# Kernel optimization log

Hardware: AMD Instinct MI355X
Metric: run time of the kernel (lower is better)

## Reference

```python
import jax, jax.numpy as jnp
import numpy as np

VOCAB = 30522
H = 100
T, B = 256, 16


def _lstm(x, W_ih, W_hh, b_ih, b_hh):
    # x: [T, B, I]; PyTorch gate order: i, f, g, o stacked in 4H rows.
    gx = jnp.einsum('tbi,gi->tbg', x, W_ih) + b_ih + b_hh  # [T, B, 4H]
    Hd = W_hh.shape[1]
    h0 = jnp.zeros((x.shape[1], Hd), x.dtype)
    c0 = jnp.zeros((x.shape[1], Hd), x.dtype)

    def step(carry, g_t):
        h, c = carry
        gates = g_t + h @ W_hh.T
        i, f, g, o = jnp.split(gates, 4, axis=-1)
        c = jax.nn.sigmoid(f) * c + jax.nn.sigmoid(i) * jnp.tanh(g)
        h = jax.nn.sigmoid(o) * jnp.tanh(c)
        return (h, c), h

    (h, c), hs = jax.lax.scan(step, (h0, c0), gx)
    return hs, (h, c)


def setup_inputs() -> dict:
    key = jax.random.key(0)
    ks = jax.random.split(key, 12)
    s = 1.0 / np.sqrt(H)
    u = lambda k, shp: jax.random.uniform(k, shp, jnp.float32, -s, s)
    return {
        'input': jax.random.randint(ks[0], (T, B), 0, VOCAB),
        'emb': jax.random.normal(ks[1], (VOCAB, H), jnp.float32),
        'enc_W_ih': u(ks[2], (4 * H, H)),
        'enc_W_hh': u(ks[3], (4 * H, H)),
        'enc_b_ih': u(ks[4], (4 * H,)),
        'enc_b_hh': u(ks[5], (4 * H,)),
        'dec_W_ih': u(ks[6], (4 * H, H)),
        'dec_W_hh': u(ks[7], (4 * H, H)),
        'dec_b_ih': u(ks[8], (4 * H,)),
        'dec_b_hh': u(ks[9], (4 * H,)),
        'out_W': u(ks[10], (VOCAB, H)),
        'out_b': u(ks[11], (VOCAB,)),
    }


def reference(input, emb, enc_W_ih, enc_W_hh, enc_b_ih, enc_b_hh,
              dec_W_ih, dec_W_hh, dec_b_ih, dec_b_hh, out_W, out_b):
    embedded = emb[input]  # [T, B, H]
    # Encoder is run in the original forward but its (hidden, cell) are unused.
    _hs, (_h, _c) = _lstm(embedded, enc_W_ih, enc_W_hh, enc_b_ih, enc_b_hh)
    dec_out, _ = _lstm(embedded, dec_W_ih, dec_W_hh, dec_b_ih, dec_b_hh)
    out = jnp.einsum('tbh,vh->tbv', dec_out, out_W) + out_b  # [T, B, VOCAB]
    return out
```

## Files before the change

kernel.cpp:

```cpp
#include <hip/hip_runtime.h>

#define HH 100
#define G4 400
#define TT 256
#define BB 16
#define TB 4096
#define VV 30522
#define GX_ROWS 8
#define PR 64

__global__ void k_tw_ih(const float* __restrict__ W, float* __restrict__ Wt) {
    int idx = blockIdx.x * blockDim.x + threadIdx.x;
    if (idx < G4 * HH) {
        int j = idx / HH, k = idx - j * HH;
        Wt[k * G4 + j] = W[idx];
    }
}

__global__ void k_tw_out(const float* __restrict__ W, float* __restrict__ Wt) {
    int v = blockIdx.x * blockDim.x + threadIdx.x;
    if (v < VV) {
        #pragma unroll 4
        for (int k = 0; k < HH; ++k) Wt[(long)k * VV + v] = W[(long)v * HH + k];
    }
}

__global__ __launch_bounds__(256) void k_gx(const int* __restrict__ tok,
                                            const float* __restrict__ emb,
                                            const float* __restrict__ WtIh,
                                            const float* __restrict__ bih,
                                            const float* __restrict__ bhh,
                                            float* __restrict__ gx) {
    __shared__ float x_s[GX_ROWS * HH];
    int tid = threadIdx.x;
    int row0 = blockIdx.x * GX_ROWS;
    for (int i = tid; i < GX_ROWS * HH; i += 256) {
        int r = i / HH, k = i - r * HH;
        x_s[i] = emb[(long)tok[row0 + r] * HH + k];
    }
    __syncthreads();
    for (int j = tid; j < G4; j += 256) {
        float bias = bih[j] + bhh[j];
        float acc[GX_ROWS];
        #pragma unroll
        for (int r = 0; r < GX_ROWS; ++r) acc[r] = bias;
        for (int k = 0; k < HH; ++k) {
            float w = WtIh[k * G4 + j];
            #pragma unroll
            for (int r = 0; r < GX_ROWS; ++r) acc[r] += w * x_s[r * HH + k];
        }
        #pragma unroll
        for (int r = 0; r < GX_ROWS; ++r) gx[(long)(row0 + r) * G4 + j] = acc[r];
    }
}

__global__ __launch_bounds__(512) void k_lstm(const float* __restrict__ gx,
                                              const float* __restrict__ Whh,
                                              float* __restrict__ dec) {
    __shared__ float h_s[HH];
    __shared__ float gates_s[G4];
    int tid = threadIdx.x;
    int b = blockIdx.x;
    float w[HH];
    if (tid < G4) {
        #pragma unroll
        for (int k = 0; k < HH; ++k) w[k] = Whh[tid * HH + k];
    }
    float c = 0.f;
    if (tid < HH) h_s[tid] = 0.f;
    __syncthreads();
    for (int t = 0; t < TT; ++t) {
        int row = t * BB + b;
        if (tid < G4) {
            float gxv = gx[(long)row * G4 + tid];
            float a0 = 0.f, a1 = 0.f, a2 = 0.f, a3 = 0.f;
            #pragma unroll
            for (int k = 0; k < HH; k += 4) {
                a0 += w[k]     * h_s[k];
                a1 += w[k + 1] * h_s[k + 1];
                a2 += w[k + 2] * h_s[k + 2];
                a3 += w[k + 3] * h_s[k + 3];
            }
            gates_s[tid] = gxv + ((a0 + a1) + (a2 + a3));
        }
        __syncthreads();
        if (tid < HH) {
            float gi = gates_s[tid];
            float gf = gates_s[HH + tid];
            float gg = gates_s[2 * HH + tid];
            float go = gates_s[3 * HH + tid];
            float si = 1.f / (1.f + expf(-gi));
            float sf = 1.f / (1.f + expf(-gf));
            float so = 1.f / (1.f + expf(-go));
            float tg = tanhf(gg);
            c = sf * c + si * tg;
            float h = so * tanhf(c);
            h_s[tid] = h;
            dec[(long)row * HH + tid] = h;
        }
        __syncthreads();
    }
}

__global__ __launch_bounds__(256) void k_proj(const float* __restrict__ dec,
                                              const float* __restrict__ Wt,
                                              const float* __restrict__ ob,
                                              float* __restrict__ out) {
    __shared__ float dec_t[HH * PR];
    int tid = threadIdx.x;
    int r0 = blockIdx.y * PR;
    for (int i = tid; i < PR * HH; i += 256) {
        int r = i / HH, k = i - r * HH;
        dec_t[k * PR + r] = dec[(long)r0 * HH + i];
    }
    __syncthreads();
    int v = blockIdx.x * 256 + tid;
    bool ok = v < VV;
    float acc[PR];
    #pragma unroll
    for (int r = 0; r < PR; ++r) acc[r] = 0.f;
    float wv = ok ? Wt[v] : 0.f;
    for (int k = 0; k < HH; ++k) {
        float wn = (ok && k + 1 < HH) ? Wt[(long)(k + 1) * VV + v] : 0.f;
        const float4* d4 = (const float4*)(&dec_t[k * PR]);
        #pragma unroll
        for (int q = 0; q < PR / 4; ++q) {
            float4 d = d4[q];
            acc[4 * q + 0] += d.x * wv;
            acc[4 * q + 1] += d.y * wv;
            acc[4 * q + 2] += d.z * wv;
            acc[4 * q + 3] += d.w * wv;
        }
        wv = wn;
    }
    if (ok) {
        float bias = ob[v];
        #pragma unroll
        for (int r = 0; r < PR; ++r)
            out[(long)(r0 + r) * VV + v] = acc[r] + bias;
    }
}

extern "C" void kernel_launch(void* const* d_in, const int* in_sizes, int n_in,
                              void* d_out, int out_size, void* d_ws, size_t ws_size,
                              hipStream_t stream) {
    const int*   tok  = (const int*)d_in[0];
    const float* emb  = (const float*)d_in[1];
    const float* dWih = (const float*)d_in[6];
    const float* dWhh = (const float*)d_in[7];
    const float* dbih = (const float*)d_in[8];
    const float* dbhh = (const float*)d_in[9];
    const float* outW = (const float*)d_in[10];
    const float* outb = (const float*)d_in[11];
    float* out = (float*)d_out;

    float* ws    = (float*)d_ws;
    float* gx    = ws;
    float* dec   = gx + (long)TB * G4;
    float* WtIh  = dec + (long)TB * HH;
    float* WtOut = WtIh + (long)HH * G4;

    k_tw_ih<<<(G4 * HH + 255) / 256, 256, 0, stream>>>(dWih, WtIh);
    k_tw_out<<<(VV + 255) / 256, 256, 0, stream>>>(outW, WtOut);
    k_gx<<<TB / GX_ROWS, 256, 0, stream>>>(tok, emb, WtIh, dbih, dbhh, gx);
    k_lstm<<<BB, 512, 0, stream>>>(gx, dWhh, dec);
    dim3 pg((VV + 255) / 256, TB / PR);
    k_proj<<<pg, 256, 0, stream>>>(dec, WtOut, outb, out);
}
```

Baseline: 1.319 ms.

## Compute output projection with split-bf16 MFMA instead of scalar FP32 FMA

The scalar FP32 output projection is replaced by a matrix-core kernel. Activations and weights are each split into bf16 high and low parts, and the product is taken as three MFMA 16x16x32 terms to approximate FP32 accuracy. The LSTM now writes padded bf16 hi/lo hidden states directly, and a prep kernel builds the padded hi/lo weight buffer in a workspace region it shares with gx. This trades a small accuracy loss and extra preprocessing for much higher throughput on the large GEMM; the output store remains strided and uncoalesced.

```diff
diff --git a/kernel.cpp b/kernel.cpp
--- a/kernel.cpp
+++ b/kernel.cpp
@@ -6,8 +6,21 @@
 #define BB 16
 #define TB 4096
 #define VV 30522
+#define VP 30528
+#define KP 128
 #define GX_ROWS 8
-#define PR 64
+
+typedef unsigned short u16;
+typedef __attribute__((ext_vector_type(8))) short s16x8;
+typedef __attribute__((ext_vector_type(4))) float f32x4;
+
+__device__ __forceinline__ u16 f2bf(float x) {
+    unsigned u = __float_as_uint(x);
+    return (u16)((u + 0x7fffu + ((u >> 16) & 1u)) >> 16);
+}
+__device__ __forceinline__ float bf2f(u16 h) {
+    return __uint_as_float((unsigned)h << 16);
+}
 
 __global__ void k_tw_ih(const float* __restrict__ W, float* __restrict__ Wt) {
     int idx = blockIdx.x * blockDim.x + threadIdx.x;
@@ -17,12 +30,23 @@
     }
 }
 
-__global__ void k_tw_out(const float* __restrict__ W, float* __restrict__ Wt) {
-    int v = blockIdx.x * blockDim.x + threadIdx.x;
-    if (v < VV) {
-        #pragma unroll 4
-        for (int k = 0; k < HH; ++k) Wt[(long)k * VV + v] = W[(long)v * HH + k];
-    }
+__global__ __launch_bounds__(256) void k_prep_w(const float* __restrict__ W,
+                                                u16* __restrict__ Bh,
+                                                u16* __restrict__ Bl) {
+    int idx = blockIdx.x * 256 + threadIdx.x;
+    int v = idx >> 4;
+    int kc = (idx & 15) * 8;
+    s16x8 vh, vl;
+    #pragma unroll
+    for (int j = 0; j < 8; ++j) {
+        int k = kc + j;
+        float x = (v < VV && k < HH) ? W[(long)v * HH + k] : 0.f;
+        u16 hi = f2bf(x);
+        vh[j] = (short)hi;
+        vl[j] = (short)f2bf(x - bf2f(hi));
+    }
+    *(s16x8*)(Bh + (long)v * KP + kc) = vh;
+    *(s16x8*)(Bl + (long)v * KP + kc) = vl;
 }
 
 __global__ __launch_bounds__(256) void k_gx(const int* __restrict__ tok,
@@ -56,7 +80,8 @@
 
 __global__ __launch_bounds__(512) void k_lstm(const float* __restrict__ gx,
                                               const float* __restrict__ Whh,
-                                              float* __restrict__ dec) {
+                                              u16* __restrict__ Ah,
+                                              u16* __restrict__ Al) {
     __shared__ float h_s[HH];
     __shared__ float gates_s[G4];
     int tid = threadIdx.x;
@@ -96,48 +121,82 @@
             c = sf * c + si * tg;
             float h = so * tanhf(c);
             h_s[tid] = h;
-            dec[(long)row * HH + tid] = h;
+            u16 hi = f2bf(h);
+            Ah[(long)row * KP + tid] = hi;
+            Al[(long)row * KP + tid] = f2bf(h - bf2f(hi));
+        } else if (tid < KP) {
+            Ah[(long)row * KP + tid] = 0;
+            Al[(long)row * KP + tid] = 0;
         }
         __syncthreads();
     }
 }
 
-__global__ __launch_bounds__(256) void k_proj(const float* __restrict__ dec,
-                                              const float* __restrict__ Wt,
-                                              const float* __restrict__ ob,
-                                              float* __restrict__ out) {
-    __shared__ float dec_t[HH * PR];
-    int tid = threadIdx.x;
-    int r0 = blockIdx.y * PR;
-    for (int i = tid; i < PR * HH; i += 256) {
-        int r = i / HH, k = i - r * HH;
-        dec_t[k * PR + r] = dec[(long)r0 * HH + i];
-    }
-    __syncthreads();
-    int v = blockIdx.x * 256 + tid;
-    bool ok = v < VV;
-    float acc[PR];
+__global__ __launch_bounds__(256) void k_proj_mfma(const u16* __restrict__ Ah,
+                                                   const u16* __restrict__ Al,
+                                                   const u16* __restrict__ Bh,
+                                                   const u16* __restrict__ Bl,
+                                                   const float* __restrict__ ob,
+                                                   float* __restrict__ out) {
+    int tid  = threadIdx.x;
+    int wid  = tid >> 6;
+    int lane = tid & 63;
+    int r    = lane & 15;
+    int ko   = (lane >> 4) * 8;
+
+    int m0 = blockIdx.y * 64 + (wid >> 1) * 32;
+    int n0 = blockIdx.x * 64 + (wid & 1) * 32;
+
+    const u16* pAh = Ah + (long)(m0 + r) * KP + ko;
+    const u16* pAl = Al + (long)(m0 + r) * KP + ko;
+    const u16* pBh = Bh + (long)(n0 + r) * KP + ko;
+    const u16* pBl = Bl + (long)(n0 + r) * KP + ko;
+
+    f32x4 acc00 = {0.f, 0.f, 0.f, 0.f};
+    f32x4 acc01 = {0.f, 0.f, 0.f, 0.f};
+    f32x4 acc10 = {0.f, 0.f, 0.f, 0.f};
+    f32x4 acc11 = {0.f, 0.f, 0.f, 0.f};
+
     #pragma unroll
-    for (int r = 0; r < PR; ++r) acc[r] = 0.f;
-    float wv = ok ? Wt[v] : 0.f;
-    for (int k = 0; k < HH; ++k) {
-        float wn = (ok && k + 1 < HH) ? Wt[(long)(k + 1) * VV + v] : 0.f;
-        const float4* d4 = (const float4*)(&dec_t[k * PR]);
-        #pragma unroll
-        for (int q = 0; q < PR / 4; ++q) {
-            float4 d = d4[q];
-            acc[4 * q + 0] += d.x * wv;
-            acc[4 * q + 1] += d.y * wv;
-            acc[4 * q + 2] += d.z * wv;
-            acc[4 * q + 3] += d.w * wv;
-        }
-        wv = wn;
-    }
-    if (ok) {
-        float bias = ob[v];
-        #pragma unroll
-        for (int r = 0; r < PR; ++r)
-            out[(long)(r0 + r) * VV + v] = acc[r] + bias;
+    for (int ks = 0; ks < 4; ++ks) {
+        int off = ks * 32;
+        s16x8 ah0 = *(const s16x8*)(pAh + off);
+        s16x8 ah1 = *(const s16x8*)(pAh + off + 16 * KP);
+        s16x8 al0 = *(const s16x8*)(pAl + off);
+        s16x8 al1 = *(const s16x8*)(pAl + off + 16 * KP);
+        s16x8 bh0 = *(const s16x8*)(pBh + off);
+        s16x8 bh1 = *(const s16x8*)(pBh + off + 16 * KP);
+        s16x8 bl0 = *(const s16x8*)(pBl + off);
+        s16x8 bl1 = *(const s16x8*)(pBl + off + 16 * KP);
+#define MM(d, a, b) d = __builtin_amdgcn_mfma_f32_16x16x32_bf16(a, b, d, 0, 0, 0)
+        MM(acc00, ah0, bh0); MM(acc00, ah0, bl0); MM(acc00, al0, bh0);
+        MM(acc01, ah0, bh1); MM(acc01, ah0, bl1); MM(acc01, al0, bh1);
+        MM(acc10, ah1, bh0); MM(acc10, ah1, bl0); MM(acc10, al1, bh0);
+        MM(acc11, ah1, bh1); MM(acc11, ah1, bl1); MM(acc11, al1, bh1);
+#undef MM
+    }
+
+    int hi4 = (lane >> 4) * 4;
+    int n_0 = n0 + r;
+    int n_1 = n0 + 16 + r;
+    bool ok0 = n_0 < VV;
+    bool ok1 = n_1 < VV;
+    float bias0 = ok0 ? ob[n_0] : 0.f;
+    float bias1 = ok1 ? ob[n_1] : 0.f;
+    long base0 = (long)(m0 + hi4) * VV;
+    long base1 = (long)(m0 + 16 + hi4) * VV;
+
+    if (ok0) {
+        #pragma unroll
+        for (int q = 0; q < 4; ++q) out[base0 + (long)q * VV + n_0] = acc00[q] + bias0;
+        #pragma unroll
+        for (int q = 0; q < 4; ++q) out[base1 + (long)q * VV + n_0] = acc10[q] + bias0;
+    }
+    if (ok1) {
+        #pragma unroll
+        for (int q = 0; q < 4; ++q) out[base0 + (long)q * VV + n_1] = acc01[q] + bias1;
+        #pragma unroll
+        for (int q = 0; q < 4; ++q) out[base1 + (long)q * VV + n_1] = acc11[q] + bias1;
     }
 }
 
@@ -154,16 +213,17 @@
     const float* outb = (const float*)d_in[11];
     float* out = (float*)d_out;
 
-    float* ws    = (float*)d_ws;
-    float* gx    = ws;
-    float* dec   = gx + (long)TB * G4;
-    float* WtIh  = dec + (long)TB * HH;
-    float* WtOut = WtIh + (long)HH * G4;
+    u16* Ah = (u16*)d_ws;
+    u16* Al = Ah + (long)TB * KP;
+    float* WtIh = (float*)(Al + (long)TB * KP);
+    char* big = (char*)(WtIh + (long)HH * G4);
+    float* gx = (float*)big;
+    u16* Bh = (u16*)big;
+    u16* Bl = Bh + (long)VP * KP;
 
     k_tw_ih<<<(G4 * HH + 255) / 256, 256, 0, stream>>>(dWih, WtIh);
-    k_tw_out<<<(VV + 255) / 256, 256, 0, stream>>>(outW, WtOut);
     k_gx<<<TB / GX_ROWS, 256, 0, stream>>>(tok, emb, WtIh, dbih, dbhh, gx);
-    k_lstm<<<BB, 512, 0, stream>>>(gx, dWhh, dec);
-    dim3 pg((VV + 255) / 256, TB / PR);
-    k_proj<<<pg, 256, 0, stream>>>(dec, WtOut, outb, out);
-}
+    k_lstm<<<BB, 512, 0, stream>>>(gx, dWhh, Ah, Al);
+    k_prep_w<<<(VP * 16) / 256, 256, 0, stream>>>(outW, Bh, Bl);
+    k_proj_mfma<<<dim3(VP / 64, TB / 64), 256, 0, stream>>>(Ah, Al, Bh, Bl, outb, out);
+}
```

Measured after the change: 1.325 ms. Within noise of the previous version (+0.4%).
